# Performance work log

Measured on AMD Instinct MI355X. Metric: run time of the kernel, lower is better.

The kernel has to match this reference:

```python
import jax, jax.numpy as jnp
import numpy as np

HIDDEN = 1024
N_HEADS = 16
HEAD_DIM = HIDDEN // N_HEADS


def _rope_tables(seq_len, dim, dtype):
    inv_freq = 1.0 / (10000.0 ** (jnp.arange(0, dim, 2, dtype=jnp.float32) / dim))
    t = jnp.arange(seq_len, dtype=jnp.float32)
    freqs = jnp.einsum('i,j->ij', t, inv_freq)          # [S, dim/2]
    emb = jnp.concatenate([freqs, freqs], axis=-1)       # [S, dim]
    cos = jnp.cos(emb)[None, :, None, :].astype(dtype)   # [1, S, 1, dim]
    sin = jnp.sin(emb)[None, :, None, :].astype(dtype)
    return cos, sin


def _rotate_half(x):
    x1, x2 = x[..., : x.shape[-1] // 2], x[..., x.shape[-1] // 2 :]
    return jnp.concatenate([-x2, x1], axis=-1)


def setup_inputs() -> dict:
    key = jax.random.key(0)
    ks = jax.random.split(key, 9)
    s = 1.0 / np.sqrt(HIDDEN)
    return {
        'x': jax.random.normal(ks[0], (2, 2048, HIDDEN), dtype=jnp.float32),
        'q_w': jax.random.uniform(ks[1], (HIDDEN, HIDDEN), jnp.float32, -s, s),
        'q_b': jax.random.uniform(ks[2], (HIDDEN,), jnp.float32, -s, s),
        'k_w': jax.random.uniform(ks[3], (HIDDEN, HIDDEN), jnp.float32, -s, s),
        'k_b': jax.random.uniform(ks[4], (HIDDEN,), jnp.float32, -s, s),
        'v_w': jax.random.uniform(ks[5], (HIDDEN, HIDDEN), jnp.float32, -s, s),
        'v_b': jax.random.uniform(ks[6], (HIDDEN,), jnp.float32, -s, s),
        'o_w': jax.random.uniform(ks[7], (HIDDEN, HIDDEN), jnp.float32, -s, s),
        'o_b': jax.random.uniform(ks[8], (HIDDEN,), jnp.float32, -s, s),
    }


def reference(x, q_w, q_b, k_w, k_b, v_w, v_b, o_w, o_b):
    B, S, _ = x.shape
    scale = HEAD_DIM ** -0.5
    # projections (torch Linear: x @ W.T + b)
    q = (x @ q_w.T + q_b).reshape(B, S, N_HEADS, HEAD_DIM)
    k = (x @ k_w.T + k_b).reshape(B, S, N_HEADS, HEAD_DIM)
    v = (x @ v_w.T + v_b).reshape(B, S, N_HEADS, HEAD_DIM)
    # RoPE
    cos, sin = _rope_tables(S, HEAD_DIM, x.dtype)
    q = q * cos + _rotate_half(q) * sin
    k = k * cos + _rotate_half(k) * sin
    # attention: [B, H, S, S]
    scores = jnp.einsum('bqhd,bkhd->bhqk', q, k) * scale
    attn = jax.nn.softmax(scores, axis=-1)
    out = jnp.einsum('bhqk,bkhd->bqhd', attn, v).reshape(B, S, HIDDEN)
    return out @ o_w.T + o_b
```

## Files before the change

kernel.cpp:

```cpp
#include <hip/hip_runtime.h>
#include <hip/hip_bf16.h>


#define SEQ    2048
#define BATCH  2
#define NHEADS 16
#define HDIM   64
#define HID    1024
#define NTOK   (BATCH*SEQ)

typedef __bf16 bf16x8 __attribute__((ext_vector_type(8)));
typedef float  f32x4  __attribute__((ext_vector_type(4)));
typedef unsigned short u16x8 __attribute__((ext_vector_type(8)));

__device__ __forceinline__ unsigned short bfc(float x) {
  return __builtin_bit_cast(unsigned short, (__bf16)x);
}
#define EXP2(x) __builtin_amdgcn_exp2f(x)

__device__ __forceinline__ void gload16(const void* gptr, void* ldsptr) {
  typedef __attribute__((address_space(3))) unsigned int as3_uint;
  typedef const __attribute__((address_space(1))) unsigned int as1_uint;
  __builtin_amdgcn_global_load_lds(
      (as1_uint*)(unsigned long long)gptr,
      (as3_uint*)(unsigned int)(unsigned long long)ldsptr,
      16, 0, 0);
}

__device__ __forceinline__ void cvt8(const float* __restrict__ s,
                                     unsigned short* __restrict__ d, int i) {
  float4 a = *reinterpret_cast<const float4*>(s + i);
  float4 b = *reinterpret_cast<const float4*>(s + i + 4);
  u16x8 o;
  o[0] = bfc(a.x); o[1] = bfc(a.y); o[2] = bfc(a.z); o[3] = bfc(a.w);
  o[4] = bfc(b.x); o[5] = bfc(b.y); o[6] = bfc(b.z); o[7] = bfc(b.w);
  *reinterpret_cast<u16x8*>(d + i) = o;
}

__global__ __launch_bounds__(256) void prep(
    const float* __restrict__ x,
    const float* __restrict__ qw, const float* __restrict__ kw,
    const float* __restrict__ vw, const float* __restrict__ ow,
    unsigned short* __restrict__ xb,
    unsigned short* __restrict__ wqb, unsigned short* __restrict__ wkb,
    unsigned short* __restrict__ wvb, unsigned short* __restrict__ wob,
    float* __restrict__ ct, float* __restrict__ st)
{
  const int XN = NTOK * HID / 8;
  const int WN = HID * HID / 8;
  int tid = blockIdx.x * 256 + threadIdx.x;
  if (tid < XN) {
    cvt8(x, xb, tid * 8);
  } else if (tid < XN + 4 * WN) {
    int r = tid - XN;
    int which = r >> 17;
    int i = (r & (WN - 1)) * 8;
    const float* s = (which == 0) ? qw : (which == 1) ? kw : (which == 2) ? vw : ow;
    unsigned short* d = (which == 0) ? wqb : (which == 1) ? wkb : (which == 2) ? wvb : wob;
    cvt8(s, d, i);
  } else {
    int idx = tid - (XN + 4 * WN);
    if (idx < SEQ * 32) {
      int p = idx >> 5, j = idx & 31;
      float inv = powf(10000.0f, -(float)(2 * j) * (1.0f / 64.0f));
      float a = (float)p * inv;
      ct[idx] = cosf(a);
      st[idx] = sinf(a);
    }
  }
}

__global__ __launch_bounds__(256) void gemm_qkv(
    const unsigned short* __restrict__ X,
    const unsigned short* __restrict__ Wq, const unsigned short* __restrict__ Wk,
    const unsigned short* __restrict__ Wv,
    const float* __restrict__ bq, const float* __restrict__ bk, const float* __restrict__ bv,
    const float* __restrict__ ct, const float* __restrict__ st,
    unsigned short* __restrict__ Qo, unsigned short* __restrict__ Ko,
    unsigned short* __restrict__ VTo)
{
  __shared__ unsigned short LSH[16384];
  const int z = blockIdx.z;
  const unsigned short* W = (z == 0) ? Wq : (z == 1) ? Wk : Wv;
  const float* bias = (z == 0) ? bq : (z == 1) ? bk : bv;
  const int tm = blockIdx.x, tn = blockIdx.y;
  const int t = threadIdx.x, w = t >> 6, l = t & 63;
  const int wm = w >> 1, wn = w & 1, g = l >> 4;

  f32x4 acc[4][4] = {};

  const int arow0 = tm * 128, brow0 = tn * 128;
  const int s0 = w * 2, s1 = w * 2 + 1;
  const int r0 = s0 * 16 + (l >> 2), r1 = s1 * 16 + (l >> 2);
  const int kc = (l & 3) * 8;

#define GSTAGE(buf, k0)                                                            \
  {                                                                                \
    gload16(X + (long)(arow0 + r0) * HID + (k0) + kc, LSH + (buf) * 4096 + s0 * 512); \
    gload16(X + (long)(arow0 + r1) * HID + (k0) + kc, LSH + (buf) * 4096 + s1 * 512); \
    gload16(W + (long)(brow0 + r0) * HID + (k0) + kc, LSH + 8192 + (buf) * 4096 + s0 * 512); \
    gload16(W + (long)(brow0 + r1) * HID + (k0) + kc, LSH + 8192 + (buf) * 4096 + s1 * 512); \
  }

  GSTAGE(0, 0)
  asm volatile("s_waitcnt vmcnt(0)" ::: "memory");
  __builtin_amdgcn_s_barrier();
  int cur = 0;
  for (int k0 = 0; k0 < HID; k0 += 32) {
    if (k0 + 32 < HID) GSTAGE(cur ^ 1, k0 + 32)
    bf16x8 af[4], bfr[4];
#pragma unroll
    for (int fm = 0; fm < 4; ++fm)
      af[fm] = *reinterpret_cast<const bf16x8*>(
          LSH + cur * 4096 + (wm * 64 + fm * 16 + (l & 15)) * 32 + g * 8);
#pragma unroll
    for (int fn = 0; fn < 4; ++fn)
      bfr[fn] = *reinterpret_cast<const bf16x8*>(
          LSH + 8192 + cur * 4096 + (wn * 64 + fn * 16 + (l & 15)) * 32 + g * 8);
    __builtin_amdgcn_s_setprio(1);
#pragma unroll
    for (int fm = 0; fm < 4; ++fm)
#pragma unroll
      for (int fn = 0; fn < 4; ++fn)
        acc[fm][fn] = __builtin_amdgcn_mfma_f32_16x16x32_bf16(af[fm], bfr[fn], acc[fm][fn], 0, 0, 0);
    __builtin_amdgcn_s_setprio(0);
    asm volatile("s_waitcnt vmcnt(0)" ::: "memory");
    __builtin_amdgcn_s_barrier();
    cur ^= 1;
  }
#undef GSTAGE

  const int colb = brow0 + wn * 64;
  float bsv[4];
#pragma unroll
  for (int fn = 0; fn < 4; ++fn) bsv[fn] = bias[colb + fn * 16 + (l & 15)];

  if (z == 2) {
#pragma unroll
    for (int fm = 0; fm < 4; ++fm) {
      int tok = wm * 64 + fm * 16 + g * 4;
#pragma unroll
      for (int fn = 0; fn < 4; ++fn) {
        int col = wn * 64 + fn * 16 + (l & 15);
        unsigned int u0 = (unsigned int)bfc(acc[fm][fn][0] + bsv[fn]) |
                          ((unsigned int)bfc(acc[fm][fn][1] + bsv[fn]) << 16);
        unsigned int u1 = (unsigned int)bfc(acc[fm][fn][2] + bsv[fn]) |
                          ((unsigned int)bfc(acc[fm][fn][3] + bsv[fn]) << 16);
        uint2 uv; uv.x = u0; uv.y = u1;
        *reinterpret_cast<uint2*>(&LSH[col * 128 + (tok ^ ((col & 7) << 3))]) = uv;
      }
    }
    __syncthreads();
    const int bb = arow0 >> 11, stok = arow0 & (SEQ - 1);
#pragma unroll
    for (int p8 = 0; p8 < 8; ++p8) {
      int col = p8 * 16 + (t >> 4);
      int soff = (t & 15) * 8;
      uint4 v = *reinterpret_cast<const uint4*>(&LSH[col * 128 + (soff ^ ((col & 7) << 3))]);
      int hh = (brow0 + col) >> 6;
      int dd = col & 63;
      unsigned short* dst = VTo + ((long)(bb * NHEADS + hh) * HDIM + dd) * SEQ + stok + soff;
      *reinterpret_cast<uint4*>(dst) = v;
    }
    return;
  }

  unsigned short* Out = (z == 0) ? Qo : Ko;
  const int h = colb >> 6;
#pragma unroll
  for (int fm = 0; fm < 4; ++fm) {
#pragma unroll
    for (int r = 0; r < 4; ++r) {
      int grow = arow0 + wm * 64 + fm * 16 + g * 4 + r;
      int b = grow >> 11, sidx = grow & (SEQ - 1);
      unsigned short* ob = Out + ((long)(b * NHEADS + h) * SEQ + sidx) * HDIM;
#pragma unroll
      for (int fn2 = 0; fn2 < 2; ++fn2) {
        int d1 = fn2 * 16 + (l & 15);
        float v1 = acc[fm][fn2][r] + bsv[fn2];
        float v2 = acc[fm][fn2 + 2][r] + bsv[fn2 + 2];
        float c = ct[sidx * 32 + d1], sn = st[sidx * 32 + d1];
        float o1 = v1 * c - v2 * sn;
        float o2 = v2 * c + v1 * sn;
        if (z == 0) { o1 *= 0.18033688f; o2 *= 0.18033688f; }
        ob[d1] = bfc(o1);
        ob[d1 + 32] = bfc(o2);
      }
    }
  }
}

__global__ __launch_bounds__(256) void attn(
    const unsigned short* __restrict__ Qb,
    const unsigned short* __restrict__ Kb,
    const unsigned short* __restrict__ VTb,
    unsigned short* __restrict__ Ob)
{
  __shared__ unsigned short Kl[2][64 * 64];
  __shared__ unsigned short Vl[3][64 * 64];
  __shared__ unsigned short Pl[4][32 * 64];
  const int bh = blockIdx.x, qt = blockIdx.y;
  const int b = bh >> 4, h = bh & 15;
  const int t = threadIdx.x, w = t >> 6, l = t & 63;
  const long hb = (long)bh * SEQ * HDIM;
  const int g = l >> 4;
  const int swz = (l & 7) << 4;

  const int q0 = qt * 128 + w * 32;
  bf16x8 qf[2][2];
#pragma unroll
  for (int f = 0; f < 2; ++f)
#pragma unroll
    for (int ks = 0; ks < 2; ++ks)
      qf[f][ks] = *reinterpret_cast<const bf16x8*>(
          Qb + hb + (long)(q0 + f * 16 + (l & 15)) * HDIM + ks * 32 + g * 8);

  f32x4 oacc[2][4] = {};
  float lrun[2] = {0.f, 0.f};

  const int rowq = (l & 15) * 128;
  const int colx0 = (g * 16) ^ swz;
  const int colx1 = (64 + g * 16) ^ swz;
  char* const Pw = (char*)Pl + w * 4096;

  const int srow = l >> 3;
  const int scol = (((l & 7) * 16) ^ ((l >> 3) << 4)) >> 1;
  const unsigned short* kp0 = Kb + hb + (long)(w * 16 + srow) * HDIM + scol;
  const unsigned short* kp1 = kp0 + 8 * HDIM;
  const unsigned short* vp0 = VTb + hb + (long)(w * 16 + srow) * SEQ + scol;
  const unsigned short* vp1 = vp0 + 8 * SEQ;

#define STAGE(kbuf, vbuf)                                              \
  {                                                                    \
    gload16(kp0, (char*)Kl + (kbuf) * 8192 + w * 2048);                \
    gload16(kp1, (char*)Kl + (kbuf) * 8192 + w * 2048 + 1024);         \
    gload16(vp0, (char*)Vl + (vbuf) * 8192 + w * 2048);                \
    gload16(vp1, (char*)Vl + (vbuf) * 8192 + w * 2048 + 1024);         \
    kp0 += 64 * HDIM; kp1 += 64 * HDIM; vp0 += 64; vp1 += 64;          \
  }

#define QK(kbuf)                                                                  \
  _Pragma("unroll")                                                               \
  for (int f = 0; f < 2; ++f)                                                     \
    _Pragma("unroll")                                                             \
    for (int fn = 0; fn < 4; ++fn) sa[f][fn] = f32x4{0.f, 0.f, 0.f, 0.f};         \
  _Pragma("unroll")                                                               \
  for (int fnK = 0; fnK < 4; ++fnK) {                                             \
    const char* kb_ = (char*)Kl + (kbuf) * 8192 + fnK * 2048 + rowq;              \
    bf16x8 kf0 = *reinterpret_cast<const bf16x8*>(kb_ + colx0);                   \
    bf16x8 kf1 = *reinterpret_cast<const bf16x8*>(kb_ + colx1);                   \
    sa[0][fnK] = __builtin_amdgcn_mfma_f32_16x16x32_bf16(kf0, qf[0][0], sa[0][fnK], 0, 0, 0); \
    sa[0][fnK] = __builtin_amdgcn_mfma_f32_16x16x32_bf16(kf1, qf[0][1], sa[0][fnK], 0, 0, 0); \
    sa[1][fnK] = __builtin_amdgcn_mfma_f32_16x16x32_bf16(kf0, qf[1][0], sa[1][fnK], 0, 0, 0); \
    sa[1][fnK] = __builtin_amdgcn_mfma_f32_16x16x32_bf16(kf1, qf[1][1], sa[1][fnK], 0, 0, 0); \
  }

#define PFREAD                                                                    \
  _Pragma("unroll")                                                               \
  for (int f = 0; f < 2; ++f) {                                                   \
    pf[f][0] = *reinterpret_cast<const bf16x8*>(Pw + f * 2048 + rowq + colx0);    \
    pf[f][1] = *reinterpret_cast<const bf16x8*>(Pw + f * 2048 + rowq + colx1);    \
  }

#define PVSTEP(vbuf)                                                              \
  _Pragma("unroll")                                                               \
  for (int fnD = 0; fnD < 4; ++fnD) {                                             \
    const char* vb_ = (char*)Vl + (vbuf) * 8192 + fnD * 2048 + rowq;              \
    bf16x8 vf0 = *reinterpret_cast<const bf16x8*>(vb_ + colx0);                   \
    bf16x8 vf1 = *reinterpret_cast<const bf16x8*>(vb_ + colx1);                   \
    oacc[0][fnD] = __builtin_amdgcn_mfma_f32_16x16x32_bf16(vf0, pf[0][0], oacc[0][fnD], 0, 0, 0); \
    oacc[0][fnD] = __builtin_amdgcn_mfma_f32_16x16x32_bf16(vf1, pf[0][1], oacc[0][fnD], 0, 0, 0); \
    oacc[1][fnD] = __builtin_amdgcn_mfma_f32_16x16x32_bf16(vf0, pf[1][0], oacc[1][fnD], 0, 0, 0); \
    oacc[1][fnD] = __builtin_amdgcn_mfma_f32_16x16x32_bf16(vf1, pf[1][1], oacc[1][fnD], 0, 0, 0); \
  }

#define SOFTPACK                                                                  \
  _Pragma("unroll")                                                               \
  for (int f = 0; f < 2; ++f) {                                                   \
    float rs = 0.f;                                                               \
    _Pragma("unroll")                                                             \
    for (int fn = 0; fn < 4; ++fn)                                                \
      _Pragma("unroll")                                                           \
      for (int r = 0; r < 4; ++r) {                                               \
        float p = EXP2(sa[f][fn][r]);                                             \
        sa[f][fn][r] = p;                                                         \
        rs += p;                                                                  \
      }                                                                           \
    lrun[f] += rs;                                                                \
    char* pw_ = Pw + f * 2048 + rowq;                                             \
    _Pragma("unroll")                                                             \
    for (int fn = 0; fn < 4; ++fn) {                                              \
      unsigned int u0 = (unsigned int)bfc(sa[f][fn][0]) | ((unsigned int)bfc(sa[f][fn][1]) << 16); \
      unsigned int u1 = (unsigned int)bfc(sa[f][fn][2]) | ((unsigned int)bfc(sa[f][fn][3]) << 16); \
      uint2 uv; uv.x = u0; uv.y = u1;                                             \
      *reinterpret_cast<uint2*>(pw_ + ((fn * 32 + g * 8) ^ swz)) = uv;            \
    }                                                                             \
  }

  f32x4 sa[2][4];
  bf16x8 pf[2][2];

  STAGE(0, 0)
  asm volatile("s_waitcnt vmcnt(0)" ::: "memory");
  __builtin_amdgcn_s_barrier();

  STAGE(1, 1)
  __builtin_amdgcn_s_setprio(1);
  QK(0)
  __builtin_amdgcn_s_setprio(0);
  SOFTPACK
  asm volatile("s_waitcnt vmcnt(0)" ::: "memory");
  __builtin_amdgcn_s_barrier();

  int kcur = 1, vr = 0, vw = 2;
  for (int it = 1; it < SEQ / 64; ++it) {
    PFREAD
    if (it + 1 < SEQ / 64) STAGE(kcur ^ 1, vw)
    __builtin_amdgcn_s_setprio(1);
    QK(kcur)
    PVSTEP(vr)
    __builtin_amdgcn_s_setprio(0);
    SOFTPACK
    asm volatile("s_waitcnt vmcnt(0)" ::: "memory");
    __builtin_amdgcn_s_barrier();
    kcur ^= 1;
    vr = (vr == 2) ? 0 : vr + 1;
    vw = (vw == 2) ? 0 : vw + 1;
  }

  PFREAD
  __builtin_amdgcn_s_setprio(1);
  PVSTEP(vr)
  __builtin_amdgcn_s_setprio(0);

#undef STAGE
#undef QK
#undef PFREAD
#undef PVSTEP
#undef SOFTPACK

#pragma unroll
  for (int f = 0; f < 2; ++f) {
    float lr = lrun[f];
    lr += __shfl_xor(lr, 16);
    lr += __shfl_xor(lr, 32);
    float inv = 1.0f / lr;
    int q = q0 + f * 16 + (l & 15);
    unsigned short* op = Ob + (long)(b * SEQ + q) * HID + h * HDIM;
#pragma unroll
    for (int fnD = 0; fnD < 4; ++fnD) {
      unsigned int lo = (unsigned int)bfc(oacc[f][fnD][0] * inv) |
                        ((unsigned int)bfc(oacc[f][fnD][1] * inv) << 16);
      unsigned int hi = (unsigned int)bfc(oacc[f][fnD][2] * inv) |
                        ((unsigned int)bfc(oacc[f][fnD][3] * inv) << 16);
      uint2 uv; uv.x = lo; uv.y = hi;
      *reinterpret_cast<uint2*>(op + fnD * 16 + g * 4) = uv;
    }
  }
}

__global__ __launch_bounds__(256) void gemm_o(
    const unsigned short* __restrict__ A,
    const unsigned short* __restrict__ W,
    const float* __restrict__ bias,
    float* __restrict__ Out)
{
  __shared__ unsigned short Al[2][128 * 32];
  __shared__ unsigned short Bl[2][64 * 32];
  const int tm = blockIdx.x, tn = blockIdx.y;
  const int t = threadIdx.x, w = t >> 6, l = t & 63;
  const int wm = w >> 1, wn = w & 1;

  f32x4 acc[4][2] = {};
  const int arow0 = tm * 128, brow0 = tn * 64;
  const int s0 = w * 2, s1 = w * 2 + 1;
  const int r0 = s0 * 16 + (l >> 2), r1 = s1 * 16 + (l >> 2);
  const int rb = w * 16 + (l >> 2);
  const int kc = (l & 3) * 8;

#define GSTAGE(buf, k0)                                                       \
  {                                                                           \
    gload16(A + (long)(arow0 + r0) * HID + (k0) + kc, Al[buf] + s0 * 512);    \
    gload16(A + (long)(arow0 + r1) * HID + (k0) + kc, Al[buf] + s1 * 512);    \
    gload16(W + (long)(brow0 + rb) * HID + (k0) + kc, Bl[buf] + w * 512);     \
  }

  GSTAGE(0, 0)
  asm volatile("s_waitcnt vmcnt(0)" ::: "memory");
  __builtin_amdgcn_s_barrier();
  int cur = 0;
  for (int k0 = 0; k0 < HID; k0 += 32) {
    if (k0 + 32 < HID) GSTAGE(cur ^ 1, k0 + 32)
    bf16x8 af[4], bfr[2];
#pragma unroll
    for (int fm = 0; fm < 4; ++fm)
      af[fm] = *reinterpret_cast<const bf16x8*>(Al[cur] + (wm * 64 + fm * 16 + (l & 15)) * 32 + (l >> 4) * 8);
#pragma unroll
    for (int fn = 0; fn < 2; ++fn)
      bfr[fn] = *reinterpret_cast<const bf16x8*>(Bl[cur] + (wn * 32 + fn * 16 + (l & 15)) * 32 + (l >> 4) * 8);
    __builtin_amdgcn_s_setprio(1);
#pragma unroll
    for (int fm = 0; fm < 4; ++fm)
#pragma unroll
      for (int fn = 0; fn < 2; ++fn)
        acc[fm][fn] = __builtin_amdgcn_mfma_f32_16x16x32_bf16(af[fm], bfr[fn], acc[fm][fn], 0, 0, 0);
    __builtin_amdgcn_s_setprio(0);
    asm volatile("s_waitcnt vmcnt(0)" ::: "memory");
    __builtin_amdgcn_s_barrier();
    cur ^= 1;
  }
#undef GSTAGE

  const int colb = brow0 + wn * 32;
  float bsv[2];
#pragma unroll
  for (int fn = 0; fn < 2; ++fn) bsv[fn] = bias[colb + fn * 16 + (l & 15)];
#pragma unroll
  for (int fm = 0; fm < 4; ++fm)
#pragma unroll
    for (int r = 0; r < 4; ++r) {
      int grow = arow0 + wm * 64 + fm * 16 + (l >> 4) * 4 + r;
#pragma unroll
      for (int fn = 0; fn < 2; ++fn)
        Out[(long)grow * HID + colb + fn * 16 + (l & 15)] = acc[fm][fn][r] + bsv[fn];
    }
}

extern "C" void kernel_launch(void* const* d_in, const int* in_sizes, int n_in,
                              void* d_out, int out_size, void* d_ws, size_t ws_size,
                              hipStream_t stream) {
  const float* x  = (const float*)d_in[0];
  const float* qw = (const float*)d_in[1];
  const float* qb = (const float*)d_in[2];
  const float* kw = (const float*)d_in[3];
  const float* kb = (const float*)d_in[4];
  const float* vw = (const float*)d_in[5];
  const float* vb = (const float*)d_in[6];
  const float* ow = (const float*)d_in[7];
  const float* ob = (const float*)d_in[8];
  float* out = (float*)d_out;

  char* p = (char*)d_ws;
  unsigned short* xb  = (unsigned short*)p; p += (size_t)NTOK * HID * 2;
  unsigned short* wqb = (unsigned short*)p; p += (size_t)HID * HID * 2;
  unsigned short* wkb = (unsigned short*)p; p += (size_t)HID * HID * 2;
  unsigned short* wvb = (unsigned short*)p; p += (size_t)HID * HID * 2;
  unsigned short* wob = (unsigned short*)p; p += (size_t)HID * HID * 2;
  unsigned short* Qb  = (unsigned short*)p; p += (size_t)NTOK * HID * 2;
  unsigned short* Kb  = (unsigned short*)p; p += (size_t)NTOK * HID * 2;
  unsigned short* VTb = (unsigned short*)p; p += (size_t)NTOK * HID * 2;
  float* ct = (float*)p; p += (size_t)SEQ * 32 * 4;
  float* st = (float*)p; p += (size_t)SEQ * 32 * 4;
  unsigned short* Ab  = xb;

  const int XN = NTOK * HID / 8, WN = HID * HID / 8;
  const int prep_threads = XN + 4 * WN + SEQ * 32;
  prep<<<dim3((prep_threads + 255) / 256), 256, 0, stream>>>(
      x, qw, kw, vw, ow, xb, wqb, wkb, wvb, wob, ct, st);

  gemm_qkv<<<dim3(NTOK / 128, HID / 128, 3), 256, 0, stream>>>(
      xb, wqb, wkb, wvb, qb, kb, vb, ct, st, Qb, Kb, VTb);

  attn<<<dim3(BATCH * NHEADS, SEQ / 128), 256, 0, stream>>>(Qb, Kb, VTb, Ab);

  gemm_o<<<dim3(NTOK / 128, HID / 64), 256, 0, stream>>>(Ab, wob, ob, out);
}
```

Before: 119.8 us.

## Triple-buffer GEMM loads and compute softmax row sums via MFMA ones column

Both projection GEMMs move from double to triple buffering with a prefetch distance of two, waiting on a partial vmcnt so that two stages of global-to-LDS loads stay in flight. In attention, the scalar per-row sum of exponentials is replaced by extra MFMAs against a ones-filled LDS tile, so the sum falls out of the matrix unit and the final cross-lane shuffles are simplified. This costs more LDS (lower occupancy risk) and extra MFMA work, and the row sum now uses bf16-rounded probabilities.

```diff
diff --git a/kernel.cpp b/kernel.cpp
--- a/kernel.cpp
+++ b/kernel.cpp
@@ -79,7 +79,7 @@
     unsigned short* __restrict__ Qo, unsigned short* __restrict__ Ko,
     unsigned short* __restrict__ VTo)
 {
-  __shared__ unsigned short LSH[16384];
+  __shared__ unsigned short LSH[24576];
   const int z = blockIdx.z;
   const unsigned short* W = (z == 0) ? Wq : (z == 1) ? Wk : Wv;
   const float* bias = (z == 0) ? bq : (z == 1) ? bk : bv;
@@ -94,20 +94,21 @@
   const int r0 = s0 * 16 + (l >> 2), r1 = s1 * 16 + (l >> 2);
   const int kc = (l & 3) * 8;
 
-#define GSTAGE(buf, k0)                                                            \
-  {                                                                                \
+#define GSTAGE(buf, k0)                                                               \
+  {                                                                                   \
     gload16(X + (long)(arow0 + r0) * HID + (k0) + kc, LSH + (buf) * 4096 + s0 * 512); \
     gload16(X + (long)(arow0 + r1) * HID + (k0) + kc, LSH + (buf) * 4096 + s1 * 512); \
-    gload16(W + (long)(brow0 + r0) * HID + (k0) + kc, LSH + 8192 + (buf) * 4096 + s0 * 512); \
-    gload16(W + (long)(brow0 + r1) * HID + (k0) + kc, LSH + 8192 + (buf) * 4096 + s1 * 512); \
+    gload16(W + (long)(brow0 + r0) * HID + (k0) + kc, LSH + 12288 + (buf) * 4096 + s0 * 512); \
+    gload16(W + (long)(brow0 + r1) * HID + (k0) + kc, LSH + 12288 + (buf) * 4096 + s1 * 512); \
   }
 
   GSTAGE(0, 0)
-  asm volatile("s_waitcnt vmcnt(0)" ::: "memory");
+  GSTAGE(1, 32)
+  asm volatile("s_waitcnt vmcnt(4)" ::: "memory");
   __builtin_amdgcn_s_barrier();
-  int cur = 0;
+  int cur = 0, stg = 2;
   for (int k0 = 0; k0 < HID; k0 += 32) {
-    if (k0 + 32 < HID) GSTAGE(cur ^ 1, k0 + 32)
+    if (k0 + 64 < HID) GSTAGE(stg, k0 + 64)
     bf16x8 af[4], bfr[4];
 #pragma unroll
     for (int fm = 0; fm < 4; ++fm)
@@ -116,7 +117,7 @@
 #pragma unroll
     for (int fn = 0; fn < 4; ++fn)
       bfr[fn] = *reinterpret_cast<const bf16x8*>(
-          LSH + 8192 + cur * 4096 + (wn * 64 + fn * 16 + (l & 15)) * 32 + g * 8);
+          LSH + 12288 + cur * 4096 + (wn * 64 + fn * 16 + (l & 15)) * 32 + g * 8);
     __builtin_amdgcn_s_setprio(1);
 #pragma unroll
     for (int fm = 0; fm < 4; ++fm)
@@ -124,9 +125,14 @@
       for (int fn = 0; fn < 4; ++fn)
         acc[fm][fn] = __builtin_amdgcn_mfma_f32_16x16x32_bf16(af[fm], bfr[fn], acc[fm][fn], 0, 0, 0);
     __builtin_amdgcn_s_setprio(0);
-    asm volatile("s_waitcnt vmcnt(0)" ::: "memory");
+    if (k0 + 64 < HID) {
+      asm volatile("s_waitcnt vmcnt(4)" ::: "memory");
+    } else {
+      asm volatile("s_waitcnt vmcnt(0)" ::: "memory");
+    }
     __builtin_amdgcn_s_barrier();
-    cur ^= 1;
+    cur = (cur == 2) ? 0 : cur + 1;
+    stg = (stg == 2) ? 0 : stg + 1;
   }
 #undef GSTAGE
 
@@ -199,6 +205,7 @@
   __shared__ unsigned short Kl[2][64 * 64];
   __shared__ unsigned short Vl[3][64 * 64];
   __shared__ unsigned short Pl[4][32 * 64];
+  __shared__ unsigned short Vext[16 * 64];
   const int bh = blockIdx.x, qt = blockIdx.y;
   const int b = bh >> 4, h = bh & 15;
   const int t = threadIdx.x, w = t >> 6, l = t & 63;
@@ -216,7 +223,7 @@
           Qb + hb + (long)(q0 + f * 16 + (l & 15)) * HDIM + ks * 32 + g * 8);
 
   f32x4 oacc[2][4] = {};
-  float lrun[2] = {0.f, 0.f};
+  f32x4 oaccE[2] = {};
 
   const int rowq = (l & 15) * 128;
   const int colx0 = (g * 16) ^ swz;
@@ -272,21 +279,19 @@
     oacc[0][fnD] = __builtin_amdgcn_mfma_f32_16x16x32_bf16(vf1, pf[0][1], oacc[0][fnD], 0, 0, 0); \
     oacc[1][fnD] = __builtin_amdgcn_mfma_f32_16x16x32_bf16(vf0, pf[1][0], oacc[1][fnD], 0, 0, 0); \
     oacc[1][fnD] = __builtin_amdgcn_mfma_f32_16x16x32_bf16(vf1, pf[1][1], oacc[1][fnD], 0, 0, 0); \
-  }
+  }                                                                               \
+  oaccE[0] = __builtin_amdgcn_mfma_f32_16x16x32_bf16(vxf0, pf[0][0], oaccE[0], 0, 0, 0); \
+  oaccE[0] = __builtin_amdgcn_mfma_f32_16x16x32_bf16(vxf1, pf[0][1], oaccE[0], 0, 0, 0); \
+  oaccE[1] = __builtin_amdgcn_mfma_f32_16x16x32_bf16(vxf0, pf[1][0], oaccE[1], 0, 0, 0); \
+  oaccE[1] = __builtin_amdgcn_mfma_f32_16x16x32_bf16(vxf1, pf[1][1], oaccE[1], 0, 0, 0);
 
 #define SOFTPACK                                                                  \
   _Pragma("unroll")                                                               \
   for (int f = 0; f < 2; ++f) {                                                   \
-    float rs = 0.f;                                                               \
     _Pragma("unroll")                                                             \
     for (int fn = 0; fn < 4; ++fn)                                                \
       _Pragma("unroll")                                                           \
-      for (int r = 0; r < 4; ++r) {                                               \
-        float p = EXP2(sa[f][fn][r]);                                             \
-        sa[f][fn][r] = p;                                                         \
-        rs += p;                                                                  \
-      }                                                                           \
-    lrun[f] += rs;                                                                \
+      for (int r = 0; r < 4; ++r) sa[f][fn][r] = EXP2(sa[f][fn][r]);              \
     char* pw_ = Pw + f * 2048 + rowq;                                             \
     _Pragma("unroll")                                                             \
     for (int fn = 0; fn < 4; ++fn) {                                              \
@@ -300,9 +305,19 @@
   f32x4 sa[2][4];
   bf16x8 pf[2][2];
 
+  {
+    int i = t * 4;
+#pragma unroll
+    for (int j = 0; j < 4; ++j)
+      Vext[i + j] = (i + j) < 64 ? (unsigned short)0x3F80 : (unsigned short)0;
+  }
+
   STAGE(0, 0)
   asm volatile("s_waitcnt vmcnt(0)" ::: "memory");
   __builtin_amdgcn_s_barrier();
+
+  const bf16x8 vxf0 = *reinterpret_cast<const bf16x8*>((char*)Vext + rowq + colx0);
+  const bf16x8 vxf1 = *reinterpret_cast<const bf16x8*>((char*)Vext + rowq + colx1);
 
   STAGE(1, 1)
   __builtin_amdgcn_s_setprio(1);
@@ -341,9 +356,7 @@
 
 #pragma unroll
   for (int f = 0; f < 2; ++f) {
-    float lr = lrun[f];
-    lr += __shfl_xor(lr, 16);
-    lr += __shfl_xor(lr, 32);
+    float lr = __shfl(oaccE[f][0], l & 15);
     float inv = 1.0f / lr;
     int q = q0 + f * 16 + (l & 15);
     unsigned short* op = Ob + (long)(b * SEQ + q) * HID + h * HDIM;
@@ -365,8 +378,8 @@
     const float* __restrict__ bias,
     float* __restrict__ Out)
 {
-  __shared__ unsigned short Al[2][128 * 32];
-  __shared__ unsigned short Bl[2][64 * 32];
+  __shared__ unsigned short Al[3][128 * 32];
+  __shared__ unsigned short Bl[3][64 * 32];
   const int tm = blockIdx.x, tn = blockIdx.y;
   const int t = threadIdx.x, w = t >> 6, l = t & 63;
   const int wm = w >> 1, wn = w & 1;
@@ -386,11 +399,12 @@
   }
 
   GSTAGE(0, 0)
-  asm volatile("s_waitcnt vmcnt(0)" ::: "memory");
+  GSTAGE(1, 32)
+  asm volatile("s_waitcnt vmcnt(3)" ::: "memory");
   __builtin_amdgcn_s_barrier();
-  int cur = 0;
+  int cur = 0, stg = 2;
   for (int k0 = 0; k0 < HID; k0 += 32) {
-    if (k0 + 32 < HID) GSTAGE(cur ^ 1, k0 + 32)
+    if (k0 + 64 < HID) GSTAGE(stg, k0 + 64)
     bf16x8 af[4], bfr[2];
 #pragma unroll
     for (int fm = 0; fm < 4; ++fm)
@@ -405,9 +419,14 @@
       for (int fn = 0; fn < 2; ++fn)
         acc[fm][fn] = __builtin_amdgcn_mfma_f32_16x16x32_bf16(af[fm], bfr[fn], acc[fm][fn], 0, 0, 0);
     __builtin_amdgcn_s_setprio(0);
-    asm volatile("s_waitcnt vmcnt(0)" ::: "memory");
+    if (k0 + 64 < HID) {
+      asm volatile("s_waitcnt vmcnt(3)" ::: "memory");
+    } else {
+      asm volatile("s_waitcnt vmcnt(0)" ::: "memory");
+    }
     __builtin_amdgcn_s_barrier();
-    cur ^= 1;
+    cur = (cur == 2) ? 0 : cur + 1;
+    stg = (stg == 2) ? 0 : stg + 1;
   }
 #undef GSTAGE
 
```

Result: faster. 114.7 us (-4.2%).
